# Kernel tuning notes

Measured on AMD Instinct MI355X. Metric: run time of the kernel, lower is better.

Reference implementation:

```python
import jax, jax.numpy as jnp
import numpy as np

E = 64          # num experts
IN = 512        # input_size
OUT = 512       # output_size
N = 131072      # total tokens = sum(expert_size)
CAP = 3072      # static per-expert capacity (>= max expert_size)


def _make_expert_sizes():
    # uneven but deterministic sizes summing to N, all <= CAP
    rng = np.random.default_rng(0)
    sizes = np.full(E, N // E, dtype=np.int32)
    d = rng.integers(0, 513, size=E // 2).astype(np.int32)
    sizes[0::2] += d
    sizes[1::2] -= d
    assert sizes.sum() == N and sizes.max() <= CAP and sizes.min() > 0
    return jnp.asarray(sizes, dtype=jnp.int32)


def setup_inputs() -> dict:
    key = jax.random.key(0)
    k1, k2 = jax.random.split(key)
    inputs = jax.random.normal(k1, (N, IN), dtype=jnp.float32)
    # matches nn.init.uniform_(weight, -1/in, 1/in)
    weight = jax.random.uniform(k2, (E, IN, OUT), dtype=jnp.float32,
                                minval=-1.0 / IN, maxval=1.0 / IN)
    expert_size = _make_expert_sizes()
    return {"inputs": inputs, "expert_size": expert_size, "weight": weight}


def reference(inputs, expert_size, weight):
    # Grouped GEMM: tokens are pre-sorted by expert; segment e is
    # inputs[offset[e]:offset[e]+expert_size[e]] @ weight[e].
    cap_ids = jnp.arange(CAP, dtype=jnp.int32)                # [CAP]
    offsets = jnp.cumsum(expert_size) - expert_size           # [E]
    idx = offsets[:, None] + cap_ids[None, :]                 # [E, CAP]
    valid = cap_ids[None, :] < expert_size[:, None]           # [E, CAP]
    idx = jnp.where(valid, idx, N)                            # invalid -> OOB (dropped)
    # gather tokens into padded per-expert blocks; invalid slots -> 0
    x = jnp.take(inputs, idx, axis=0, mode='fill', fill_value=0.0)  # [E, CAP, IN]
    h = jnp.einsum('eci,eio->eco', x, weight)                 # [E, CAP, OUT]
    out = jnp.zeros((N, OUT), dtype=inputs.dtype)
    out = out.at[idx.reshape(-1)].add(h.reshape(-1, OUT), mode='drop')
    return out
```

## Files before the change

kernel.cpp:

```cpp
#include <hip/hip_runtime.h>
#include <hip/hip_bf16.h>

#define E_NUM 64
#define IN_SZ 512
#define OUT_SZ 512
#define N_TOK 131072
#define CAP 3072

#define BM 128
#define BN 128
#define BK 32
#define THREADS 256
#define RT_MAX 24
#define CT_NUM 4

typedef __attribute__((ext_vector_type(8))) short short8;
typedef __attribute__((ext_vector_type(4))) float f32x4;

__device__ inline unsigned short f2bf(float f) {
    unsigned int u = __float_as_uint(f);
    unsigned int r = (u + 0x7FFF + ((u >> 16) & 1)) >> 16;
    return (unsigned short)r;
}

#define GLOAD_LDS16(g, l)                                                     \
    __builtin_amdgcn_global_load_lds(                                         \
        (const __attribute__((address_space(1))) void*)(g),                   \
        (__attribute__((address_space(3))) void*)(l), 16, 0, 0)

__global__ void offsets_kernel(const int* __restrict__ sizes, int* __restrict__ offs) {
    int e = threadIdx.x;
    int s = 0;
    for (int i = 0; i < e; ++i) s += sizes[i];
    offs[e] = s;
}

__global__ __launch_bounds__(256) void prep_wt(const float* __restrict__ W,
                                               unsigned short* __restrict__ WT) {
    __shared__ float t[32][33];
    int k0 = blockIdx.x * 32, n0 = blockIdx.y * 32, e = blockIdx.z;
    const float* We = W + (size_t)e * IN_SZ * OUT_SZ;
    int tid = threadIdx.x;
    int r = tid >> 3, c4 = (tid & 7) * 4;
    float4 v = *(const float4*)(We + (size_t)(k0 + r) * OUT_SZ + n0 + c4);
    t[r][c4 + 0] = v.x; t[r][c4 + 1] = v.y; t[r][c4 + 2] = v.z; t[r][c4 + 3] = v.w;
    __syncthreads();
    ushort4 o;
    o.x = f2bf(t[c4 + 0][r]);
    o.y = f2bf(t[c4 + 1][r]);
    o.z = f2bf(t[c4 + 2][r]);
    o.w = f2bf(t[c4 + 3][r]);
    unsigned short* O = WT + (size_t)e * IN_SZ * OUT_SZ + (size_t)(n0 + r) * IN_SZ + k0 + c4;
    *(ushort4*)O = o;
}

__global__ __launch_bounds__(THREADS, 2) void gemm_moe(
    const float* __restrict__ A, const int* __restrict__ sizes,
    const unsigned short* __restrict__ WT, const int* __restrict__ offs,
    float* __restrict__ out)
{
    int b0 = blockIdx.x;
    int wg = (b0 & 7) * 768 + (b0 >> 3);
    int ct = wg & 3;
    int rt = (wg >> 2) % RT_MAX;
    int e  = wg / (RT_MAX * CT_NUM);

    int size_e = sizes[e];
    int rows0 = rt * BM;
    if (rows0 >= size_e) return;
    int off_e = offs[e];
    int rows_rem = size_e - rows0;
    int maxr = (rows_rem < BM ? rows_rem : BM) - 1;

    __shared__ unsigned short lsA[2][BM * BK];
    __shared__ unsigned short lsB[2][BN * BK];

    int tid = threadIdx.x, l = tid & 63, w = tid >> 6;
    const char* WTe = (const char*)(WT + (size_t)e * IN_SZ * OUT_SZ);
    const float* Abase = A + (size_t)(off_e + rows0) * IN_SZ;

    float4 ar[4];

    auto loadA = [&](int kt) {
        #pragma unroll
        for (int i = 0; i < 4; ++i) {
            int idx = tid + THREADS * i;
            int row = idx >> 3, c4 = idx & 7;
            int gr = row <= maxr ? row : maxr;
            ar[i] = *(const float4*)(Abase + (size_t)gr * IN_SZ + kt * BK + c4 * 4);
        }
    };
    auto writeA = [&](int buf) {
        #pragma unroll
        for (int i = 0; i < 4; ++i) {
            int idx = tid + THREADS * i;
            ushort4 p;
            p.x = f2bf(ar[i].x); p.y = f2bf(ar[i].y);
            p.z = f2bf(ar[i].z); p.w = f2bf(ar[i].w);
            *(ushort4*)&lsA[buf][idx * 4] = p;
        }
    };
    auto stageB = [&](int buf, int kt) {
        #pragma unroll
        for (int i = 0; i < 2; ++i) {
            int j = (w * 2 + i) * 1024 + l * 16;
            int n = j >> 6, koff = j & 63;
            const char* g = WTe + (size_t)(ct * BN + n) * (IN_SZ * 2) + kt * 64 + koff;
            GLOAD_LDS16(g, &lsB[buf][(w * 2 + i) * 512]);
        }
    };

    loadA(0);
    stageB(0, 0);
    writeA(0);
    __syncthreads();

    f32x4 acc[4][4] = {};
    int wm = (w >> 1) * 64, wn = (w & 1) * 64;
    int lrow = l & 15, lk = (l >> 4) * 8;

    for (int kt = 0; kt < IN_SZ / BK; ++kt) {
        int cur = kt & 1;
        if (kt < IN_SZ / BK - 1) {
            loadA(kt + 1);
            stageB(cur ^ 1, kt + 1);
        }
        short8 af[4], bfr[4];
        #pragma unroll
        for (int m = 0; m < 4; ++m)
            af[m] = *(const short8*)&lsA[cur][(wm + m * 16 + lrow) * BK + lk];
        #pragma unroll
        for (int n = 0; n < 4; ++n)
            bfr[n] = *(const short8*)&lsB[cur][(wn + n * 16 + lrow) * BK + lk];
        #pragma unroll
        for (int m = 0; m < 4; ++m)
            #pragma unroll
            for (int n = 0; n < 4; ++n)
                acc[m][n] = __builtin_amdgcn_mfma_f32_16x16x32_bf16(af[m], bfr[n], acc[m][n], 0, 0, 0);
        if (kt < IN_SZ / BK - 1)
            writeA(cur ^ 1);
        __syncthreads();
    }

    float* outb = out + (size_t)(off_e + rows0) * OUT_SZ + ct * BN + wn;
    #pragma unroll
    for (int m = 0; m < 4; ++m) {
        #pragma unroll
        for (int j = 0; j < 4; ++j) {
            int rl = wm + m * 16 + (l >> 4) * 4 + j;
            if (rl < rows_rem) {
                float* po = outb + (size_t)rl * OUT_SZ + (l & 15);
                #pragma unroll
                for (int n = 0; n < 4; ++n)
                    po[n * 16] = acc[m][n][j];
            }
        }
    }
}

extern "C" void kernel_launch(void* const* d_in, const int* in_sizes, int n_in,
                              void* d_out, int out_size, void* d_ws, size_t ws_size,
                              hipStream_t stream) {
    const float* A      = (const float*)d_in[0];
    const int* sizes    = (const int*)d_in[1];
    const float* W      = (const float*)d_in[2];
    float* out          = (float*)d_out;

    unsigned short* WT  = (unsigned short*)d_ws;
    int* offs           = (int*)((char*)d_ws + (size_t)E_NUM * IN_SZ * OUT_SZ * 2);

    offsets_kernel<<<1, E_NUM, 0, stream>>>(sizes, offs);
    prep_wt<<<dim3(IN_SZ / 32, OUT_SZ / 32, E_NUM), 256, 0, stream>>>(W, WT);
    gemm_moe<<<E_NUM * RT_MAX * CT_NUM, THREADS, 0, stream>>>(A, sizes, WT, offs, out);
}
```

Baseline: 203.9 us.

## Widen GEMM N-tile to 256 and XOR-swizzle LDS layouts for A and B

Doubles the output-column tile per workgroup (BN 128→256, two column tiles per expert row-tile), so each fp32 A tile is loaded and converted to bf16 half as often. Each wave now holds a 64x128 accumulator. It also adds an XOR swizzle on the LDS layout of both A (on write) and B (on the global-to-LDS source address), so MFMA fragment reads avoid bank conflicts. In exchange, accumulator registers double, which may lower occupancy below the launch-bounds target or cause spills, and the grid has half as many workgroups.

Result: faster. 197.7 us (-3.0%).

```diff
diff --git a/kernel.cpp b/kernel.cpp
--- a/kernel.cpp
+++ b/kernel.cpp
@@ -8,11 +8,11 @@
 #define CAP 3072
 
 #define BM 128
-#define BN 128
+#define BN 256
 #define BK 32
 #define THREADS 256
 #define RT_MAX 24
-#define CT_NUM 4
+#define CT_NUM 2
 
 typedef __attribute__((ext_vector_type(8))) short short8;
 typedef __attribute__((ext_vector_type(4))) float f32x4;
@@ -60,9 +60,9 @@
     float* __restrict__ out)
 {
     int b0 = blockIdx.x;
-    int wg = (b0 & 7) * 768 + (b0 >> 3);
-    int ct = wg & 3;
-    int rt = (wg >> 2) % RT_MAX;
+    int wg = (b0 & 7) * (E_NUM * RT_MAX * CT_NUM / 8) + (b0 >> 3);
+    int ct = wg & (CT_NUM - 1);
+    int rt = (wg >> 1) % RT_MAX;
     int e  = wg / (RT_MAX * CT_NUM);
 
     int size_e = sizes[e];
@@ -94,19 +94,22 @@
         #pragma unroll
         for (int i = 0; i < 4; ++i) {
             int idx = tid + THREADS * i;
+            int row = idx >> 3, cb = (idx & 7) * 8;
+            int cbs = cb ^ ((((row >> 1) & 3)) << 4);
             ushort4 p;
             p.x = f2bf(ar[i].x); p.y = f2bf(ar[i].y);
             p.z = f2bf(ar[i].z); p.w = f2bf(ar[i].w);
-            *(ushort4*)&lsA[buf][idx * 4] = p;
+            *(ushort4*)((char*)&lsA[buf][0] + row * 64 + cbs) = p;
         }
     };
     auto stageB = [&](int buf, int kt) {
         #pragma unroll
-        for (int i = 0; i < 2; ++i) {
-            int j = (w * 2 + i) * 1024 + l * 16;
-            int n = j >> 6, koff = j & 63;
-            const char* g = WTe + (size_t)(ct * BN + n) * (IN_SZ * 2) + kt * 64 + koff;
-            GLOAD_LDS16(g, &lsB[buf][(w * 2 + i) * 512]);
+        for (int i = 0; i < 4; ++i) {
+            int j = (w * 4 + i) * 1024 + l * 16;
+            int n = j >> 6, c = j & 63;
+            int csrc = c ^ ((((n >> 1) & 3)) << 4);
+            const char* g = WTe + (size_t)(ct * BN + n) * (IN_SZ * 2) + kt * 64 + csrc;
+            GLOAD_LDS16(g, &lsB[buf][(w * 4 + i) * 512]);
         }
     };
 
@@ -115,9 +118,10 @@
     writeA(0);
     __syncthreads();
 
-    f32x4 acc[4][4] = {};
-    int wm = (w >> 1) * 64, wn = (w & 1) * 64;
-    int lrow = l & 15, lk = (l >> 4) * 8;
+    f32x4 acc[4][8] = {};
+    int wm = (w >> 1) * 64, wn = (w & 1) * 128;
+    int lrow = l & 15;
+    int cb = ((l >> 4) * 16) ^ ((((lrow >> 1) & 3)) << 4);
 
     for (int kt = 0; kt < IN_SZ / BK; ++kt) {
         int cur = kt & 1;
@@ -125,18 +129,25 @@
             loadA(kt + 1);
             stageB(cur ^ 1, kt + 1);
         }
-        short8 af[4], bfr[4];
+        const char* pA = (const char*)&lsA[cur][0];
+        const char* pB = (const char*)&lsB[cur][0];
+        short8 af[4];
         #pragma unroll
         for (int m = 0; m < 4; ++m)
-            af[m] = *(const short8*)&lsA[cur][(wm + m * 16 + lrow) * BK + lk];
+            af[m] = *(const short8*)(pA + (wm + m * 16 + lrow) * 64 + cb);
         #pragma unroll
-        for (int n = 0; n < 4; ++n)
-            bfr[n] = *(const short8*)&lsB[cur][(wn + n * 16 + lrow) * BK + lk];
-        #pragma unroll
-        for (int m = 0; m < 4; ++m)
+        for (int nh = 0; nh < 2; ++nh) {
+            short8 bfr[4];
             #pragma unroll
-            for (int n = 0; n < 4; ++n)
-                acc[m][n] = __builtin_amdgcn_mfma_f32_16x16x32_bf16(af[m], bfr[n], acc[m][n], 0, 0, 0);
+            for (int n2 = 0; n2 < 4; ++n2)
+                bfr[n2] = *(const short8*)(pB + (wn + nh * 64 + n2 * 16 + lrow) * 64 + cb);
+            #pragma unroll
+            for (int m = 0; m < 4; ++m)
+                #pragma unroll
+                for (int n2 = 0; n2 < 4; ++n2)
+                    acc[m][nh * 4 + n2] = __builtin_amdgcn_mfma_f32_16x16x32_bf16(
+                        af[m], bfr[n2], acc[m][nh * 4 + n2], 0, 0, 0);
+        }
         if (kt < IN_SZ / BK - 1)
             writeA(cur ^ 1);
         __syncthreads();
@@ -151,7 +162,7 @@
             if (rl < rows_rem) {
                 float* po = outb + (size_t)rl * OUT_SZ + (l & 15);
                 #pragma unroll
-                for (int n = 0; n < 4; ++n)
+                for (int n = 0; n < 8; ++n)
                     po[n * 16] = acc[m][n][j];
             }
         }
```

## Widen GEMM tile to 128x256 with 8 waves, triple-buffered LDS and swizzle

Applied to the files above, without the earlier changes.

Doubles the N tile to 256 and the block to 512 threads, so each A tile is converted and staged once per two column tiles instead of four. The A and B tiles move to a three-stage LDS ring with explicit vmcnt/lgkmcnt waits and raw s_barrier, keeping two k-steps of loads in flight. An XOR swizzle on LDS rows is meant to cut bank conflicts, and setprio raises wave priority around the MFMA block. The cost is more LDS per block (72KB) and likely lower occupancy, and correctness depends on the hand-counted waitcnt values.

Result: slower. 243.8 us (+19.6%).

```diff
diff --git a/kernel.cpp b/kernel.cpp
--- a/kernel.cpp
+++ b/kernel.cpp
@@ -8,11 +8,12 @@
 #define CAP 3072
 
 #define BM 128
-#define BN 128
+#define BN 256
 #define BK 32
-#define THREADS 256
+#define THREADS 512
 #define RT_MAX 24
-#define CT_NUM 4
+#define CT_NUM 2
+#define JT 16
 
 typedef __attribute__((ext_vector_type(8))) short short8;
 typedef __attribute__((ext_vector_type(4))) float f32x4;
@@ -60,9 +61,9 @@
     float* __restrict__ out)
 {
     int b0 = blockIdx.x;
-    int wg = (b0 & 7) * 768 + (b0 >> 3);
-    int ct = wg & 3;
-    int rt = (wg >> 2) % RT_MAX;
+    int wg = (b0 & 7) * (E_NUM * RT_MAX * CT_NUM / 8) + (b0 >> 3);
+    int ct = wg & (CT_NUM - 1);
+    int rt = (wg >> 1) % RT_MAX;
     int e  = wg / (RT_MAX * CT_NUM);
 
     int size_e = sizes[e];
@@ -72,75 +73,105 @@
     int rows_rem = size_e - rows0;
     int maxr = (rows_rem < BM ? rows_rem : BM) - 1;
 
-    __shared__ unsigned short lsA[2][BM * BK];
-    __shared__ unsigned short lsB[2][BN * BK];
+    __shared__ unsigned short lsA[3][BM * BK];
+    __shared__ unsigned short lsB[3][BN * BK];
 
     int tid = threadIdx.x, l = tid & 63, w = tid >> 6;
     const char* WTe = (const char*)(WT + (size_t)e * IN_SZ * OUT_SZ);
     const float* Abase = A + (size_t)(off_e + rows0) * IN_SZ;
 
-    float4 ar[4];
-
-    auto loadA = [&](int kt) {
-        #pragma unroll
-        for (int i = 0; i < 4; ++i) {
-            int idx = tid + THREADS * i;
-            int row = idx >> 3, c4 = idx & 7;
-            int gr = row <= maxr ? row : maxr;
-            ar[i] = *(const float4*)(Abase + (size_t)gr * IN_SZ + kt * BK + c4 * 4);
-        }
+    int arow = tid >> 2;
+    int garow = arow <= maxr ? arow : maxr;
+    const float* aptr = Abase + (size_t)garow * IN_SZ + (tid & 3) * 8;
+    int awaddr = arow * 64 + (((tid & 3) * 16) ^ ((arow & 3) << 4));
+
+    int bsrc_col = ((l & 3) * 16) ^ (((l >> 2) & 3) << 4);
+    int brow_l = l >> 2;
+
+    float4 ar[2][2];
+
+    auto loadA = [&](int kt, int p) {
+        ar[p][0] = *(const float4*)(aptr + kt * BK);
+        ar[p][1] = *(const float4*)(aptr + kt * BK + 4);
     };
-    auto writeA = [&](int buf) {
-        #pragma unroll
-        for (int i = 0; i < 4; ++i) {
-            int idx = tid + THREADS * i;
-            ushort4 p;
-            p.x = f2bf(ar[i].x); p.y = f2bf(ar[i].y);
-            p.z = f2bf(ar[i].z); p.w = f2bf(ar[i].w);
-            *(ushort4*)&lsA[buf][idx * 4] = p;
-        }
+    auto writeA = [&](int buf, int p) {
+        short8 pk;
+        pk[0] = (short)f2bf(ar[p][0].x); pk[1] = (short)f2bf(ar[p][0].y);
+        pk[2] = (short)f2bf(ar[p][0].z); pk[3] = (short)f2bf(ar[p][0].w);
+        pk[4] = (short)f2bf(ar[p][1].x); pk[5] = (short)f2bf(ar[p][1].y);
+        pk[6] = (short)f2bf(ar[p][1].z); pk[7] = (short)f2bf(ar[p][1].w);
+        *(short8*)((char*)&lsA[buf][0] + awaddr) = pk;
     };
     auto stageB = [&](int buf, int kt) {
         #pragma unroll
         for (int i = 0; i < 2; ++i) {
-            int j = (w * 2 + i) * 1024 + l * 16;
-            int n = j >> 6, koff = j & 63;
-            const char* g = WTe + (size_t)(ct * BN + n) * (IN_SZ * 2) + kt * 64 + koff;
-            GLOAD_LDS16(g, &lsB[buf][(w * 2 + i) * 512]);
+            int c = w * 2 + i;
+            int row = c * 16 + brow_l;
+            const char* g = WTe + (size_t)(ct * BN + row) * (IN_SZ * 2) + kt * 64 + bsrc_col;
+            GLOAD_LDS16(g, &lsB[buf][c * 512]);
         }
     };
 
-    loadA(0);
+    int wm = (w >> 2) * 64, wn = (w & 3) * 64;
+    int lrow = l & 15;
+    int cb = ((l >> 4) * 16) ^ ((l & 3) << 4);
+
+    f32x4 acc[4][4] = {};
+
+    #define FRAGS_AND_MFMA(buf)                                               \
+        {                                                                     \
+            const char* pA = (const char*)&lsA[buf][0];                       \
+            const char* pB = (const char*)&lsB[buf][0];                       \
+            short8 af[4], bfr[4];                                             \
+            _Pragma("unroll")                                                 \
+            for (int m = 0; m < 4; ++m)                                       \
+                af[m] = *(const short8*)(pA + (wm + m * 16 + lrow) * 64 + cb);\
+            _Pragma("unroll")                                                 \
+            for (int n = 0; n < 4; ++n)                                       \
+                bfr[n] = *(const short8*)(pB + (wn + n * 16 + lrow) * 64 + cb);\
+            asm volatile("s_waitcnt lgkmcnt(0)" ::: "memory");                \
+            __builtin_amdgcn_sched_barrier(0);                                \
+            __builtin_amdgcn_s_setprio(1);                                    \
+            _Pragma("unroll")                                                 \
+            for (int m = 0; m < 4; ++m)                                       \
+                _Pragma("unroll")                                             \
+                for (int n = 0; n < 4; ++n)                                   \
+                    acc[m][n] = __builtin_amdgcn_mfma_f32_16x16x32_bf16(      \
+                        af[m], bfr[n], acc[m][n], 0, 0, 0);                   \
+            __builtin_amdgcn_s_setprio(0);                                    \
+        }
+
+    loadA(0, 0);
     stageB(0, 0);
-    writeA(0);
-    __syncthreads();
-
-    f32x4 acc[4][4] = {};
-    int wm = (w >> 1) * 64, wn = (w & 1) * 64;
-    int lrow = l & 15, lk = (l >> 4) * 8;
-
-    for (int kt = 0; kt < IN_SZ / BK; ++kt) {
-        int cur = kt & 1;
-        if (kt < IN_SZ / BK - 1) {
-            loadA(kt + 1);
-            stageB(cur ^ 1, kt + 1);
-        }
-        short8 af[4], bfr[4];
-        #pragma unroll
-        for (int m = 0; m < 4; ++m)
-            af[m] = *(const short8*)&lsA[cur][(wm + m * 16 + lrow) * BK + lk];
-        #pragma unroll
-        for (int n = 0; n < 4; ++n)
-            bfr[n] = *(const short8*)&lsB[cur][(wn + n * 16 + lrow) * BK + lk];
-        #pragma unroll
-        for (int m = 0; m < 4; ++m)
-            #pragma unroll
-            for (int n = 0; n < 4; ++n)
-                acc[m][n] = __builtin_amdgcn_mfma_f32_16x16x32_bf16(af[m], bfr[n], acc[m][n], 0, 0, 0);
-        if (kt < IN_SZ / BK - 1)
-            writeA(cur ^ 1);
-        __syncthreads();
+    loadA(1, 1);
+    stageB(1, 1);
+    writeA(0, 0);
+    asm volatile("s_waitcnt vmcnt(4)" ::: "memory");
+    __builtin_amdgcn_sched_barrier(0);
+    asm volatile("s_waitcnt lgkmcnt(0)" ::: "memory");
+    __builtin_amdgcn_s_barrier();
+    __builtin_amdgcn_sched_barrier(0);
+
+    #pragma unroll
+    for (int j = 0; j < JT - 2; ++j) {
+        loadA(j + 2, j & 1);
+        stageB((j + 2) % 3, j + 2);
+        writeA((j + 1) % 3, (j + 1) & 1);
+        FRAGS_AND_MFMA(j % 3);
+        asm volatile("s_waitcnt vmcnt(4)" ::: "memory");
+        __builtin_amdgcn_sched_barrier(0);
+        __builtin_amdgcn_s_barrier();
+        __builtin_amdgcn_sched_barrier(0);
     }
+
+    writeA((JT - 1) % 3, (JT - 1) & 1);
+    FRAGS_AND_MFMA((JT - 2) % 3);
+    asm volatile("s_waitcnt vmcnt(0)" ::: "memory");
+    __builtin_amdgcn_sched_barrier(0);
+    __builtin_amdgcn_s_barrier();
+    __builtin_amdgcn_sched_barrier(0);
+
+    FRAGS_AND_MFMA((JT - 1) % 3);
 
     float* outb = out + (size_t)(off_e + rows0) * OUT_SZ + ct * BN + wn;
     #pragma unroll
@@ -149,7 +180,7 @@
         for (int j = 0; j < 4; ++j) {
             int rl = wm + m * 16 + (l >> 4) * 4 + j;
             if (rl < rows_rem) {
-                float* po = outb + (size_t)rl * OUT_SZ + (l & 15);
+                float* po = outb + (size_t)rl * OUT_SZ + lrow;
                 #pragma unroll
                 for (int n = 0; n < 4; ++n)
                     po[n * 16] = acc[m][n][j];
```
